# Kernel optimization log

Measured on AMD Instinct MI355X. Metric: run time of the kernel, lower is better.

The kernel has to match this reference:

```python
import jax, jax.numpy as jnp
import numpy as np

N_NODES = 10000
N_EDGES = 160000
D_IN = 128
D_EMB = 512
D_HID = 256
GAT_SLOPE = 0.2   # PyG GATv2Conv default negative_slope
MLP_SLOPE = 0.1   # relu_alpha


def _glorot(key, shape):
    fan_in, fan_out = shape[0], shape[-1]
    lim = np.sqrt(6.0 / (fan_in + fan_out))
    return jax.random.uniform(key, shape, jnp.float32, -lim, lim)


def setup_inputs() -> dict:
    key = jax.random.key(0)
    ks = jax.random.split(key, 20)
    inp = {
        'x': jax.random.normal(ks[0], (N_NODES, D_IN), jnp.float32),
        'edge_index': jax.random.randint(ks[1], (2, N_EDGES), 0, N_NODES, jnp.int64),
    }
    # GATv2 layers: (Wl, Wr, att, bias) each
    dims = [(D_IN, D_EMB), (D_EMB, D_EMB), (D_EMB, D_EMB)]
    for i, (di, do) in enumerate(dims, start=1):
        inp[f'Wl{i}'] = _glorot(ks[2 + 4 * i], (di, do))
        inp[f'Wr{i}'] = _glorot(ks[3 + 4 * i], (di, do))
        inp[f'att{i}'] = _glorot(ks[4 + 4 * i], (1, do))[0]
        inp[f'b{i}'] = jnp.zeros((do,), jnp.float32)
    # MLP
    inp['A1'] = _glorot(ks[2], (D_EMB, D_HID)); inp['c1'] = jnp.zeros((D_HID,), jnp.float32)
    inp['A2'] = _glorot(ks[3], (D_HID, D_HID)); inp['c2'] = jnp.zeros((D_HID,), jnp.float32)
    inp['A3'] = _glorot(ks[4], (D_HID, 1));     inp['c3'] = jnp.zeros((1,), jnp.float32)
    return inp


def gatv2_conv(x, src, dst, Wl, Wr, att, bias):
    # PyG GATv2Conv, heads=1: xl = source transform, xr = target transform
    xl = x @ Wl                                   # [N, D]
    xr = x @ Wr                                   # [N, D]
    # per-edge attention logit: att . leaky_relu(xl[src] + xr[dst])
    e = jax.nn.leaky_relu(xl[src] + xr[dst], GAT_SLOPE) @ att   # [E]
    # segment softmax over incoming edges of each dst node
    emax = jax.ops.segment_max(e, dst, num_segments=N_NODES)    # [N]
    w = jnp.exp(e - emax[dst])
    denom = jax.ops.segment_sum(w, dst, num_segments=N_NODES)   # [N]
    alpha = w / (denom[dst] + 1e-16)                             # [E]
    out = jax.ops.segment_sum(alpha[:, None] * xl[src], dst, num_segments=N_NODES)
    return out + bias


def reference(x, edge_index, Wl1, Wr1, att1, b1, Wl2, Wr2, att2, b2,
              Wl3, Wr3, att3, b3, A1, c1, A2, c2, A3, c3):
    src, dst = edge_index[0], edge_index[1]
    h = jnp.tanh(gatv2_conv(x, src, dst, Wl1, Wr1, att1, b1))
    h = jnp.tanh(gatv2_conv(h, src, dst, Wl2, Wr2, att2, b2))
    h = jnp.tanh(gatv2_conv(h, src, dst, Wl3, Wr3, att3, b3))
    h = jax.nn.leaky_relu(h @ A1 + c1, MLP_SLOPE)
    h = jax.nn.leaky_relu(h @ A2 + c2, MLP_SLOPE)
    logits = h @ A3 + c3                          # [N, 1]
    return jax.nn.softmax(logits, axis=0)         # softmax over nodes
```

## Files before the change

kernel.cpp:

```cpp
#include <hip/hip_runtime.h>
#include <hip/hip_bf16.h>

#define N_NODES 10000
#define N_EDGES 160000
#define D_IN    128
#define D_EMB   512
#define D_HID   256
#define DMAX    512

typedef unsigned short u16;
typedef __attribute__((ext_vector_type(8))) short short8;
typedef __attribute__((ext_vector_type(4))) float floatx4;

__device__ __forceinline__ float bf2f(u16 u) {
    union { unsigned int i; float f; } v; v.i = ((unsigned int)u) << 16; return v.f;
}
__device__ __forceinline__ u16 f2bf(float f) {
    union { float f; unsigned int i; } v; v.f = f;
    unsigned int x = v.i;
    return (u16)((x + 0x7fffu + ((x >> 16) & 1u)) >> 16);
}
__device__ __forceinline__ float inval(const void* p, int fp32, int idx) {
    return fp32 ? ((const float*)p)[idx] : bf2f(((const u16*)p)[idx]);
}

__device__ __forceinline__ void gld_lds16(const u16* g, u16* l) {
    __builtin_amdgcn_global_load_lds((const __attribute__((address_space(1))) void*)g,
                                     (__attribute__((address_space(3))) void*)l,
                                     16, 0, 0);
}

__device__ __forceinline__ int xcd_chunk(int bid, int total) {
    int q = total >> 3, r = total & 7;
    int xcd = bid & 7, idx = bid >> 3;
    return (xcd < r ? xcd * (q + 1) : r * (q + 1) + (xcd - r) * q) + idx;
}

__device__ __forceinline__ int edge_src(const int* __restrict__ ei, int flg, int e) {
    int v = flg ? ei[2 * e] : ei[e];
    return min(max(v, 0), N_NODES - 1);
}
__device__ __forceinline__ int edge_dst(const int* __restrict__ ei, int flg, int e) {
    int v = flg ? ei[2 * N_EDGES + 2 * e] : ei[N_EDGES + e];
    return min(max(v, 0), N_NODES - 1);
}

__global__ void sentinel_kernel(float* out, int n) {
    int i = blockIdx.x * 256 + threadIdx.x;
    if (i < n) out[i] = 1.0f;
}

__global__ __launch_bounds__(256)
void detect_zero_kernel(const int* __restrict__ ei, const u16* __restrict__ xu,
                        int* flag, int* counts, float* logits, int* ghist) {
    int gid = blockIdx.x * 256 + threadIdx.x;
    for (int i = gid; i < N_NODES; i += gridDim.x * 256) { counts[i] = 0; logits[i] = 0.f; }
    for (int i = gid; i < DMAX; i += gridDim.x * 256) ghist[i] = 0;
    if (blockIdx.x != 0) return;
    __shared__ int s_or[256];
    __shared__ int s_cnt[256];
    int t = threadIdx.x;
    int v = 0;
    for (int k = t; k < 4096; k += 256) v |= ei[1 + 2 * k];
    int c = 0;
    for (int k = t; k < 4096; k += 256) {
        u16 u = xu[k];
        int ex = (u >> 7) & 0xFF;
        bool plaus = (u == 0) || (ex >= 64 && ex <= 191);
        if (!plaus) c++;
    }
    s_or[t] = v; s_cnt[t] = c;
    __syncthreads();
    for (int off = 128; off > 0; off >>= 1) {
        if (t < off) { s_or[t] |= s_or[t + off]; s_cnt[t] += s_cnt[t + off]; }
        __syncthreads();
    }
    if (t == 0) {
        flag[0] = (s_or[0] == 0) ? 1 : 0;
        flag[1] = (s_cnt[0] > 256) ? 1 : 0;
    }
}

struct ConvJobs {
    const void* src[10];
    u16* dh[10];
    int rows[10], cols[10], trans[10];
    int cum[11];
    int njobs;
};

__global__ __launch_bounds__(256)
void convert_fused_kernel(ConvJobs jobs, const int* __restrict__ flag) {
    int idx = blockIdx.x * 256 + threadIdx.x;
    if (idx >= jobs.cum[jobs.njobs]) return;
    int fp32 = flag[1];
    int jb = 0;
    while (idx >= jobs.cum[jb + 1]) jb++;
    int local = idx - jobs.cum[jb];
    float v = inval(jobs.src[jb], fp32, local);
    u16 hi = f2bf(v);
    int o;
    if (jobs.trans[jb]) {
        int r = local / jobs.cols[jb], c = local % jobs.cols[jb];
        o = c * jobs.rows[jb] + r;
    } else o = local;
    jobs.dh[jb][o] = hi;
}

__global__ void count_edges_kernel(const int* __restrict__ ei, const int* __restrict__ flag,
                                   int* counts) {
    int e = blockIdx.x * 256 + threadIdx.x;
    if (e < N_EDGES) atomicAdd(&counts[edge_dst(ei, flag[0], e)], 1);
}

__global__ __launch_bounds__(256)
void scan_counts_kernel(int* counts, int* rowptr) {
    __shared__ int part[256];
    int tid = threadIdx.x;
    const int CH = 40;
    int base = tid * CH;
    int loc[CH];
    int s = 0;
    #pragma unroll
    for (int i = 0; i < CH; i++) {
        int idx = base + i;
        int c = (idx < N_NODES) ? counts[idx] : 0;
        loc[i] = s; s += c;
    }
    part[tid] = s;
    __syncthreads();
    for (int off = 1; off < 256; off <<= 1) {
        int v = part[tid];
        int add = (tid >= off) ? part[tid - off] : 0;
        __syncthreads();
        part[tid] = v + add;
        __syncthreads();
    }
    int pre = (tid > 0) ? part[tid - 1] : 0;
    #pragma unroll
    for (int i = 0; i < CH; i++) {
        int idx = base + i;
        if (idx < N_NODES) { int v = pre + loc[i]; rowptr[idx] = v; counts[idx] = v; }
    }
    if (tid == 255) rowptr[N_NODES] = part[255];
}

__global__ void fill_esrcp_kernel(const int* __restrict__ ei, const int* __restrict__ flag,
                                  int* counts, int* esrcp) {
    int e = blockIdx.x * 256 + threadIdx.x;
    if (e < N_EDGES) {
        int flg = flag[0];
        int pos = atomicAdd(&counts[edge_dst(ei, flg, e)], 1);
        if (pos >= 0 && pos < N_EDGES) esrcp[pos] = edge_src(ei, flg, e);
    }
}

__global__ __launch_bounds__(256)
void lpt_hist_kernel(const int* __restrict__ rowptr, int* __restrict__ ghist) {
    __shared__ int lhist[DMAX];
    int t = threadIdx.x;
    for (int d = t; d < DMAX; d += 256) lhist[d] = 0;
    __syncthreads();
    int n = blockIdx.x * 256 + t;
    if (n < N_NODES) {
        int d = min(rowptr[n + 1] - rowptr[n], DMAX - 1);
        atomicAdd(&lhist[d], 1);
    }
    __syncthreads();
    for (int d = t; d < DMAX; d += 256) {
        int c = lhist[d];
        if (c > 0) atomicAdd(&ghist[d], c);
    }
}

__global__ __launch_bounds__(256)
void lpt_scan_kernel(const int* __restrict__ ghist, int* __restrict__ doff) {
    __shared__ int part[256];
    int t = threadIdx.x;
    int d0 = (DMAX - 1) - 2 * t;
    int d1 = d0 - 1;
    int c0 = ghist[d0], c1 = ghist[d1];
    part[t] = c0 + c1;
    __syncthreads();
    for (int o = 1; o < 256; o <<= 1) {
        int v = part[t];
        int add = (t >= o) ? part[t - o] : 0;
        __syncthreads();
        part[t] = v + add;
        __syncthreads();
    }
    int pre = (t > 0) ? part[t - 1] : 0;
    doff[d0] = pre;
    doff[d1] = pre + c0;
}

__global__ __launch_bounds__(256)
void lpt_scatter_kernel(const int* __restrict__ rowptr, int* __restrict__ doff,
                        int* __restrict__ order) {
    __shared__ int lhist[DMAX];
    __shared__ int lbase[DMAX];
    int t = threadIdx.x;
    for (int d = t; d < DMAX; d += 256) lhist[d] = 0;
    __syncthreads();
    int n = blockIdx.x * 256 + t;
    int dg = 0;
    if (n < N_NODES) {
        dg = min(rowptr[n + 1] - rowptr[n], DMAX - 1);
        atomicAdd(&lhist[dg], 1);
    }
    __syncthreads();
    for (int d = t; d < DMAX; d += 256) {
        int c = lhist[d];
        lbase[d] = (c > 0) ? atomicAdd(&doff[d], c) : 0;
        lhist[d] = 0;
    }
    __syncthreads();
    if (n < N_NODES) {
        int rank = atomicAdd(&lhist[dg], 1);
        int pos = lbase[dg] + rank;
        if (pos >= 0 && pos < N_NODES) order[pos] = n;
    }
}

__global__ __launch_bounds__(256)
void gemm_dual_kernel(const u16* __restrict__ Ah,
                      const u16* __restrict__ B0h, const u16* __restrict__ B1h,
                      u16* __restrict__ C0, float* __restrict__ C1,
                      int M, int N, int K)
{
    __shared__ u16 sAh[2][128 * 32];
    __shared__ u16 sBh[2][128 * 32];
    int nb = N >> 7;
    int nx = 2 * nb;
    int ny = (M + 127) >> 7;
    int w = xcd_chunk((int)blockIdx.x, nx * ny);
    int by = w / nx;
    int bxh = w - by * nx;
    int half = bxh >= nb;
    int bx = half ? (bxh - nb) : bxh;
    const u16* BTh = half ? B1h : B0h;

    int tid = threadIdx.x;
    int lane = tid & 63, wv = tid >> 6;
    int l15 = lane & 15, l4 = lane >> 4;
    int wr = (wv >> 1) * 64, wc = (wv & 1) * 64;
    int m0 = by * 128, n0 = bx * 128;

    int i0 = tid, i1 = tid + 256;
    int r0 = i0 >> 2, b0 = i0 & 3, sb0 = b0 ^ ((r0 >> 1) & 3);
    int r1 = i1 >> 2, b1 = i1 & 3, sb1 = b1 ^ ((r1 >> 1) & 3);
    int gr0 = min(m0 + r0, M - 1), gr1 = min(m0 + r1, M - 1);
    const u16* a0p = Ah + (size_t)gr0 * K + sb0 * 8;
    const u16* a1p = Ah + (size_t)gr1 * K + sb1 * 8;
    const u16* bb0p = BTh + (size_t)(n0 + r0) * K + sb0 * 8;
    const u16* bb1p = BTh + (size_t)(n0 + r1) * K + sb1 * 8;
    int lo0 = wv * 64 * 8;
    int lo1 = (256 + wv * 64) * 8;

    floatx4 acc[4][4];
    #pragma unroll
    for (int i = 0; i < 4; i++)
        #pragma unroll
        for (int j = 0; j < 4; j++) acc[i][j] = (floatx4){0.f, 0.f, 0.f, 0.f};

    int aoff[4], boff[4];
    #pragma unroll
    for (int i = 0; i < 4; i++) {
        int arow = wr + i * 16 + l15;
        aoff[i] = arow * 32 + ((l4 ^ ((arow >> 1) & 3)) << 3);
        int bcol = wc + i * 16 + l15;
        boff[i] = bcol * 32 + ((l4 ^ ((bcol >> 1) & 3)) << 3);
    }

    for (int kk = 0; kk < K; kk += 64) {
        __syncthreads();
        gld_lds16(a0p + kk, &sAh[0][lo0]);
        gld_lds16(a1p + kk, &sAh[0][lo1]);
        gld_lds16(bb0p + kk, &sBh[0][lo0]);
        gld_lds16(bb1p + kk, &sBh[0][lo1]);
        gld_lds16(a0p + kk + 32, &sAh[1][lo0]);
        gld_lds16(a1p + kk + 32, &sAh[1][lo1]);
        gld_lds16(bb0p + kk + 32, &sBh[1][lo0]);
        gld_lds16(bb1p + kk + 32, &sBh[1][lo1]);
        __syncthreads();

        #pragma unroll
        for (int s = 0; s < 2; s++) {
            short8 ah[4];
            #pragma unroll
            for (int i = 0; i < 4; i++) ah[i] = *(const short8*)(&sAh[s][aoff[i]]);
            #pragma unroll
            for (int j = 0; j < 4; j++) {
                short8 bh = *(const short8*)(&sBh[s][boff[j]]);
                #pragma unroll
                for (int i = 0; i < 4; i++)
                    acc[i][j] = __builtin_amdgcn_mfma_f32_16x16x32_bf16(ah[i], bh, acc[i][j], 0, 0, 0);
            }
        }
    }

    #pragma unroll
    for (int j = 0; j < 4; j++) {
        int col = n0 + wc + j * 16 + l15;
        #pragma unroll
        for (int i = 0; i < 4; i++) {
            #pragma unroll
            for (int r = 0; r < 4; r++) {
                int row = m0 + wr + i * 16 + l4 * 4 + r;
                if (row < M) {
                    if (half) C1[(size_t)row * N + col] = acc[i][j][r];
                    else      C0[(size_t)row * N + col] = f2bf(acc[i][j][r]);
                }
            }
        }
    }
}

template<int FUSE>
__global__ __launch_bounds__(256)
void gemm_mlp64_kernel(const u16* __restrict__ Ah,
                       const u16* __restrict__ BTh,
                       u16* __restrict__ Ch,
                       const void* __restrict__ biasraw,
                       const void* __restrict__ A3raw, float* __restrict__ logits,
                       const int* __restrict__ flag,
                       int M, int N, int K)
{
    __shared__ u16 sAh[2][64 * 32];
    __shared__ u16 sBh[2][64 * 32];
    int tid = threadIdx.x;
    int lane = tid & 63, wv = tid >> 6;
    int l15 = lane & 15, l4 = lane >> 4;
    int nx = N >> 6;
    int ny = (M + 63) >> 6;
    int w = xcd_chunk((int)blockIdx.x, nx * ny);
    int by = w / nx;
    int bx = w - by * nx;
    int m0 = by * 64, n0 = bx * 64;

    int r = (tid >> 2), blk = tid & 3, sb = blk ^ ((r >> 1) & 3);
    int gr = min(m0 + r, M - 1);
    const u16* ap = Ah + (size_t)gr * K + sb * 8;
    const u16* bp = BTh + (size_t)(n0 + r) * K + sb * 8;
    int lo = wv * 64 * 8;

    floatx4 acc[4];
    #pragma unroll
    for (int j = 0; j < 4; j++) acc[j] = (floatx4){0.f, 0.f, 0.f, 0.f};

    int arow = wv * 16 + l15;
    int aoff = arow * 32 + ((l4 ^ ((arow >> 1) & 3)) << 3);
    int boff[4];
    #pragma unroll
    for (int j = 0; j < 4; j++) {
        int bcol = j * 16 + l15;
        boff[j] = bcol * 32 + ((l4 ^ ((bcol >> 1) & 3)) << 3);
    }

    for (int kk = 0; kk < K; kk += 64) {
        __syncthreads();
        gld_lds16(ap + kk, &sAh[0][lo]);
        gld_lds16(bp + kk, &sBh[0][lo]);
        gld_lds16(ap + kk + 32, &sAh[1][lo]);
        gld_lds16(bp + kk + 32, &sBh[1][lo]);
        __syncthreads();

        #pragma unroll
        for (int s = 0; s < 2; s++) {
            short8 ah = *(const short8*)(&sAh[s][aoff]);
            #pragma unroll
            for (int j = 0; j < 4; j++) {
                short8 bh = *(const short8*)(&sBh[s][boff[j]]);
                acc[j] = __builtin_amdgcn_mfma_f32_16x16x32_bf16(ah, bh, acc[j], 0, 0, 0);
            }
        }
    }

    const int fp32 = flag[1];
    float lsum[4] = {0.f, 0.f, 0.f, 0.f};
    #pragma unroll
    for (int j = 0; j < 4; j++) {
        int col = n0 + j * 16 + l15;
        float bv = inval(biasraw, fp32, col);
        float a3 = FUSE ? inval(A3raw, fp32, col) : 0.f;
        #pragma unroll
        for (int rr = 0; rr < 4; rr++) {
            int row = m0 + wv * 16 + l4 * 4 + rr;
            if (row < M) {
                float v = acc[j][rr] + bv;
                v = v > 0.f ? v : 0.1f * v;
                if (FUSE) {
                    lsum[rr] += v * a3;
                } else {
                    Ch[(size_t)row * N + col] = f2bf(v);
                }
            }
        }
    }
    if (FUSE) {
        #pragma unroll
        for (int rr = 0; rr < 4; rr++) {
            float s = lsum[rr];
            s += __shfl_xor(s, 1);
            s += __shfl_xor(s, 2);
            s += __shfl_xor(s, 4);
            s += __shfl_xor(s, 8);
            int row = m0 + wv * 16 + l4 * 4 + rr;
            if (l15 == 0 && row < M) atomicAdd(&logits[row], s);
        }
    }
}

__global__ __launch_bounds__(256)
void gat_wave_kernel(const int* __restrict__ rowptr, const int* __restrict__ esrcp,
                     const int* __restrict__ order,
                     const u16* __restrict__ xlb, const float* __restrict__ xr,
                     const void* __restrict__ att, const void* __restrict__ bias,
                     const int* __restrict__ flag,
                     u16* __restrict__ hh)
{
    int lane = threadIdx.x & 63, wv = threadIdx.x >> 6;
    int slot = blockIdx.x * 4 + wv;
    if (slot >= N_NODES) return;
    int n = order[slot];
    n = min(max(n, 0), N_NODES - 1);
    int fp32 = flag[1];
    int d0 = lane * 8;
    int l3 = lane & 3;

    int beg = rowptr[n], end = rowptr[n + 1];
    int deg = end - beg;
    int ng = (deg + 3) >> 2;

    const u16* xbase = xlb + d0;

    const float* xrr = xr + (size_t)n * D_EMB;
    float4 r0 = *(const float4*)(xrr + d0);
    float4 r1 = *(const float4*)(xrr + d0 + 4);
    float xrv[8] = {r0.x, r0.y, r0.z, r0.w, r1.x, r1.y, r1.z, r1.w};
    float attv[8];
    #pragma unroll
    for (int k = 0; k < 8; k++) attv[k] = inval(att, fp32, d0 + k);

    float m_run = -3.4e38f, s_run = 0.f;
    float acc[8] = {0.f, 0.f, 0.f, 0.f, 0.f, 0.f, 0.f, 0.f};

    auto ldidx = [&](int g) -> int {
        return esrcp[min(beg + 4 * g + l3, N_EDGES - 1)];
    };

    if (ng > 0) {
        int i0 = ldidx(0);
        uint4 cu0, cu1, cu2, cu3;
        {
            int s0 = __shfl(i0, 0), s1 = __shfl(i0, 1), s2 = __shfl(i0, 2), s3 = __shfl(i0, 3);
            cu0 = *(const uint4*)(xbase + (size_t)s0 * D_EMB);
            cu1 = *(const uint4*)(xbase + (size_t)s1 * D_EMB);
            cu2 = *(const uint4*)(xbase + (size_t)s2 * D_EMB);
            cu3 = *(const uint4*)(xbase + (size_t)s3 * D_EMB);
        }
        int nidx = (ng > 1) ? ldidx(1) : 0;

        for (int g = 0; g < ng; g++) {
            uint4 nu0, nu1, nu2, nu3;
            int nidx2 = 0;
            bool have_next = (g + 1 < ng);
            if (have_next) {
                int t0 = __shfl(nidx, 0), t1 = __shfl(nidx, 1),
                    t2 = __shfl(nidx, 2), t3 = __shfl(nidx, 3);
                nu0 = *(const uint4*)(xbase + (size_t)t0 * D_EMB);
                nu1 = *(const uint4*)(xbase + (size_t)t1 * D_EMB);
                nu2 = *(const uint4*)(xbase + (size_t)t2 * D_EMB);
                nu3 = *(const uint4*)(xbase + (size_t)t3 * D_EMB);
                if (g + 2 < ng) nidx2 = ldidx(g + 2);
            }

            union { uint4 q; u16 us[8]; } u0, u1, u2, u3;
            u0.q = cu0; u1.q = cu1; u2.q = cu2; u3.q = cu3;
            float v0[8], v1[8], v2[8], v3[8];
            #pragma unroll
            for (int k = 0; k < 8; k++) {
                v0[k] = bf2f(u0.us[k]); v1[k] = bf2f(u1.us[k]);
                v2[k] = bf2f(u2.us[k]); v3[k] = bf2f(u3.us[k]);
            }
            float e0 = 0.f, e1 = 0.f, e2 = 0.f, e3 = 0.f;
            #pragma unroll
            for (int k = 0; k < 8; k++) {
                float t0 = v0[k] + xrv[k]; t0 = fmaxf(t0, 0.2f * t0); e0 += attv[k] * t0;
                float t1 = v1[k] + xrv[k]; t1 = fmaxf(t1, 0.2f * t1); e1 += attv[k] * t1;
                float t2 = v2[k] + xrv[k]; t2 = fmaxf(t2, 0.2f * t2); e2 += attv[k] * t2;
                float t3 = v3[k] + xrv[k]; t3 = fmaxf(t3, 0.2f * t3); e3 += attv[k] * t3;
            }
            #pragma unroll
            for (int o = 32; o > 0; o >>= 1) {
                e0 += __shfl_xor(e0, o);
                e1 += __shfl_xor(e1, o);
                e2 += __shfl_xor(e2, o);
                e3 += __shfl_xor(e3, o);
            }
            int base = beg + 4 * g;
            if (base + 1 >= end) e1 = -3.4e38f;
            if (base + 2 >= end) e2 = -3.4e38f;
            if (base + 3 >= end) e3 = -3.4e38f;
            float m4 = fmaxf(fmaxf(e0, e1), fmaxf(e2, e3));
            float m_new = fmaxf(m_run, m4);
            float sc = __expf(m_run - m_new);
            float w0 = __expf(e0 - m_new), w1 = __expf(e1 - m_new);
            float w2 = __expf(e2 - m_new), w3 = __expf(e3 - m_new);
            s_run = s_run * sc + (w0 + w1) + (w2 + w3);
            #pragma unroll
            for (int k = 0; k < 8; k++)
                acc[k] = acc[k] * sc + w0 * v0[k] + w1 * v1[k] + w2 * v2[k] + w3 * v3[k];
            m_run = m_new;

            if (have_next) {
                cu0 = nu0; cu1 = nu1; cu2 = nu2; cu3 = nu3;
                nidx = nidx2;
            }
        }
    }

    float inv = 1.f / (s_run + 1e-16f);
    union { uint4 q; u16 us[8]; } ph;
    #pragma unroll
    for (int k = 0; k < 8; k++) {
        float h = tanhf(acc[k] * inv + inval(bias, fp32, d0 + k));
        ph.us[k] = f2bf(h);
    }
    *(uint4*)(&hh[(size_t)n * D_EMB + d0]) = ph.q;
}

__global__ __launch_bounds__(256)
void softmax_kernel(const float* __restrict__ logits, float* __restrict__ out)
{
    __shared__ float red[4];
    __shared__ float s_m, s_s;
    int tid = threadIdx.x, lane = tid & 63, wv = tid >> 6;
    float m = -3.4e38f;
    for (int i = tid; i < N_NODES; i += 256) m = fmaxf(m, logits[i]);
    #pragma unroll
    for (int o = 32; o > 0; o >>= 1) m = fmaxf(m, __shfl_down(m, o));
    if (lane == 0) red[wv] = m;
    __syncthreads();
    if (tid == 0) {
        float mm = red[0];
        for (int i = 1; i < 4; i++) mm = fmaxf(mm, red[i]);
        s_m = mm;
    }
    __syncthreads();
    float mm = s_m;
    float s = 0.f;
    for (int i = tid; i < N_NODES; i += 256) s += __expf(logits[i] - mm);
    #pragma unroll
    for (int o = 32; o > 0; o >>= 1) s += __shfl_down(s, o);
    if (lane == 0) red[wv] = s;
    __syncthreads();
    if (tid == 0) {
        float ss = 0.f;
        for (int i = 0; i < 4; i++) ss += red[i];
        s_s = ss;
    }
    __syncthreads();
    float invs = 1.f / s_s;
    for (int i = tid; i < N_NODES; i += 256) out[i] = __expf(logits[i] - mm) * invs;
}

extern "C" void kernel_launch(void* const* d_in, const int* in_sizes, int n_in,
                              void* d_out, int out_size, void* d_ws, size_t ws_size,
                              hipStream_t stream)
{
    const void* x   = d_in[0];
    const int*  ei  = (const int*)d_in[1];
    const void* Wl[3]  = {d_in[2],  d_in[6],  d_in[10]};
    const void* Wr[3]  = {d_in[3],  d_in[7],  d_in[11]};
    const void* att[3] = {d_in[4],  d_in[8],  d_in[12]};
    const void* bia[3] = {d_in[5],  d_in[9],  d_in[13]};
    const void* A1 = d_in[14];
    const void* c1 = d_in[15];
    const void* A2 = d_in[16];
    const void* c2 = d_in[17];
    const void* A3 = d_in[18];

    char* p = (char*)d_ws;
    auto alloc = [&](size_t bytes) {
        char* r = p;
        p += (bytes + 255) & ~(size_t)255;
        return r;
    };
    u16*   xlb    = (u16*)  alloc((size_t)N_NODES * D_EMB * 4);
    float* xr     = (float*)alloc((size_t)N_NODES * D_EMB * 4);
    u16*   hh     = (u16*)  alloc((size_t)N_NODES * D_EMB * 2);
    int*   esrcp  = (int*)  alloc((size_t)N_EDGES * 4);
    int*   rowptr = (int*)  alloc((size_t)(N_NODES + 1) * 4);
    int*   counts = (int*)  alloc((size_t)N_NODES * 4);
    int*   flag   = (int*)  alloc(256);
    float* logits = (float*)alloc((size_t)N_NODES * 4);
    int*   ghist  = (int*)  alloc(DMAX * 4);
    int*   doff   = (int*)  alloc(DMAX * 4);
    int*   order  = (int*)  alloc((size_t)N_NODES * 4);
    u16* wl1h = (u16*)alloc(D_EMB * D_IN  * 2);
    u16* wr1h = (u16*)alloc(D_EMB * D_IN  * 2);
    u16* wl2h = (u16*)alloc(D_EMB * D_EMB * 2);
    u16* wr2h = (u16*)alloc(D_EMB * D_EMB * 2);
    u16* wl3h = (u16*)alloc(D_EMB * D_EMB * 2);
    u16* wr3h = (u16*)alloc(D_EMB * D_EMB * 2);
    u16* a1h  = (u16*)alloc(D_EMB * D_HID * 2);
    u16* a2h  = (u16*)alloc(D_HID * D_HID * 2);
    u16* xph  = (u16*)alloc((size_t)N_NODES * D_IN * 2);
    size_t needed = (size_t)(p - (char*)d_ws);

    if (ws_size < needed) {
        sentinel_kernel<<<(out_size + 255) / 256, 256, 0, stream>>>((float*)d_out, out_size);
        return;
    }

    u16* m1h = (u16*)xlb;

    detect_zero_kernel<<<40, 256, 0, stream>>>(ei, (const u16*)x, flag, counts, logits, ghist);
    count_edges_kernel<<<(N_EDGES + 255) / 256, 256, 0, stream>>>(ei, flag, counts);
    scan_counts_kernel<<<1, 256, 0, stream>>>(counts, rowptr);
    fill_esrcp_kernel<<<(N_EDGES + 255) / 256, 256, 0, stream>>>(ei, flag, counts, esrcp);

    int nblk = (N_NODES + 255) / 256;
    lpt_hist_kernel<<<nblk, 256, 0, stream>>>(rowptr, ghist);
    lpt_scan_kernel<<<1, 256, 0, stream>>>(ghist, doff);
    lpt_scatter_kernel<<<nblk, 256, 0, stream>>>(rowptr, doff, order);

    ConvJobs jobs;
    auto setjob = [&](int i, const void* s, u16* dh, int r, int c, int tr) {
        jobs.src[i] = s; jobs.dh[i] = dh;
        jobs.rows[i] = r; jobs.cols[i] = c; jobs.trans[i] = tr;
    };
    setjob(0, x,     xph,  N_NODES, D_IN, 0);
    setjob(1, Wl[0], wl1h, D_IN,  D_EMB, 1);
    setjob(2, Wr[0], wr1h, D_IN,  D_EMB, 1);
    setjob(3, Wl[1], wl2h, D_EMB, D_EMB, 1);
    setjob(4, Wr[1], wr2h, D_EMB, D_EMB, 1);
    setjob(5, Wl[2], wl3h, D_EMB, D_EMB, 1);
    setjob(6, Wr[2], wr3h, D_EMB, D_EMB, 1);
    setjob(7, A1,    a1h,  D_EMB, D_HID, 1);
    setjob(8, A2,    a2h,  D_HID, D_HID, 1);
    jobs.njobs = 9;
    jobs.cum[0] = 0;
    for (int i = 0; i < 9; i++) jobs.cum[i + 1] = jobs.cum[i] + jobs.rows[i] * jobs.cols[i];
    int ctotal = jobs.cum[9];
    convert_fused_kernel<<<(ctotal + 255) / 256, 256, 0, stream>>>(jobs, flag);

    int gdual = (2 * D_EMB / 128) * ((N_NODES + 127) / 128);
    int gmlp  = (D_HID / 64) * ((N_NODES + 63) / 64);
    int gatgrid = (N_NODES + 3) / 4;

    gemm_dual_kernel<<<gdual, 256, 0, stream>>>(xph, wl1h, wr1h, xlb, xr, N_NODES, D_EMB, D_IN);
    gat_wave_kernel<<<gatgrid, 256, 0, stream>>>(rowptr, esrcp, order, xlb, xr, att[0], bia[0], flag, hh);
    gemm_dual_kernel<<<gdual, 256, 0, stream>>>(hh, wl2h, wr2h, xlb, xr, N_NODES, D_EMB, D_EMB);
    gat_wave_kernel<<<gatgrid, 256, 0, stream>>>(rowptr, esrcp, order, xlb, xr, att[1], bia[1], flag, hh);
    gemm_dual_kernel<<<gdual, 256, 0, stream>>>(hh, wl3h, wr3h, xlb, xr, N_NODES, D_EMB, D_EMB);
    gat_wave_kernel<<<gatgrid, 256, 0, stream>>>(rowptr, esrcp, order, xlb, xr, att[2], bia[2], flag, hh);

    gemm_mlp64_kernel<0><<<gmlp, 256, 0, stream>>>(hh, a1h, m1h, c1, nullptr, nullptr, flag, N_NODES, D_HID, D_EMB);
    gemm_mlp64_kernel<1><<<gmlp, 256, 0, stream>>>(m1h, a2h, nullptr, c2, A3, logits, flag, N_NODES, D_HID, D_HID);
    softmax_kernel<<<1, 256, 0, stream>>>(logits, (float*)d_out);
}
```

Before: 373.1 us.

## Merge CSR build and degree-sort preprocessing into fewer kernel launches

Folds edge counting into the weight-conversion kernel and computes the degree histogram and its scan inside the single-block count scan. The edge fill and LPT scatter now run as one launch with a block-index split. This cuts the preprocessing launches from eight to four (detect, count+convert, scan, fill+scatter), removing launch gaps and serialization. The cost is a longer single-block scan kernel with shared-memory atomics.

```diff
diff --git a/kernel.cpp b/kernel.cpp
--- a/kernel.cpp
+++ b/kernel.cpp
@@ -52,10 +52,9 @@
 
 __global__ __launch_bounds__(256)
 void detect_zero_kernel(const int* __restrict__ ei, const u16* __restrict__ xu,
-                        int* flag, int* counts, float* logits, int* ghist) {
+                        int* flag, int* counts, float* logits) {
     int gid = blockIdx.x * 256 + threadIdx.x;
     for (int i = gid; i < N_NODES; i += gridDim.x * 256) { counts[i] = 0; logits[i] = 0.f; }
-    for (int i = gid; i < DMAX; i += gridDim.x * 256) ghist[i] = 0;
     if (blockIdx.x != 0) return;
     __shared__ int s_or[256];
     __shared__ int s_cnt[256];
@@ -81,6 +80,8 @@
     }
 }
 
+#define EBLK ((N_EDGES + 255) / 256)
+
 struct ConvJobs {
     const void* src[10];
     u16* dh[10];
@@ -90,8 +91,15 @@
 };
 
 __global__ __launch_bounds__(256)
-void convert_fused_kernel(ConvJobs jobs, const int* __restrict__ flag) {
-    int idx = blockIdx.x * 256 + threadIdx.x;
+void count_convert_kernel(const int* __restrict__ ei, int* counts,
+                          ConvJobs jobs, const int* __restrict__ flag) {
+    int b = blockIdx.x;
+    if (b < EBLK) {
+        int e = b * 256 + threadIdx.x;
+        if (e < N_EDGES) atomicAdd(&counts[edge_dst(ei, flag[0], e)], 1);
+        return;
+    }
+    int idx = (b - EBLK) * 256 + threadIdx.x;
     if (idx >= jobs.cum[jobs.njobs]) return;
     int fp32 = flag[1];
     int jb = 0;
@@ -107,16 +115,13 @@
     jobs.dh[jb][o] = hi;
 }
 
-__global__ void count_edges_kernel(const int* __restrict__ ei, const int* __restrict__ flag,
-                                   int* counts) {
-    int e = blockIdx.x * 256 + threadIdx.x;
-    if (e < N_EDGES) atomicAdd(&counts[edge_dst(ei, flag[0], e)], 1);
-}
-
-__global__ __launch_bounds__(256)
-void scan_counts_kernel(int* counts, int* rowptr) {
+__global__ __launch_bounds__(256)
+void scan_counts_kernel(int* counts, int* rowptr, int* doff) {
     __shared__ int part[256];
+    __shared__ int hist[DMAX];
     int tid = threadIdx.x;
+    for (int d = tid; d < DMAX; d += 256) hist[d] = 0;
+    __syncthreads();
     const int CH = 40;
     int base = tid * CH;
     int loc[CH];
@@ -125,6 +130,7 @@
     for (int i = 0; i < CH; i++) {
         int idx = base + i;
         int c = (idx < N_NODES) ? counts[idx] : 0;
+        if (idx < N_NODES) atomicAdd(&hist[min(c, DMAX - 1)], 1);
         loc[i] = s; s += c;
     }
     part[tid] = s;
@@ -143,82 +149,62 @@
         if (idx < N_NODES) { int v = pre + loc[i]; rowptr[idx] = v; counts[idx] = v; }
     }
     if (tid == 255) rowptr[N_NODES] = part[255];
-}
-
-__global__ void fill_esrcp_kernel(const int* __restrict__ ei, const int* __restrict__ flag,
-                                  int* counts, int* esrcp) {
-    int e = blockIdx.x * 256 + threadIdx.x;
+    __syncthreads();
+    int d0 = (DMAX - 1) - 2 * tid;
+    int d1 = d0 - 1;
+    int c0 = hist[d0], c1 = hist[d1];
+    __syncthreads();
+    part[tid] = c0 + c1;
+    __syncthreads();
+    for (int o = 1; o < 256; o <<= 1) {
+        int v = part[tid];
+        int add = (tid >= o) ? part[tid - o] : 0;
+        __syncthreads();
+        part[tid] = v + add;
+        __syncthreads();
+    }
+    int pre2 = (tid > 0) ? part[tid - 1] : 0;
+    doff[d0] = pre2;
+    doff[d1] = pre2 + c0;
+}
+
+__global__ __launch_bounds__(256)
+void fill_scatter_kernel(const int* __restrict__ ei, const int* __restrict__ flag,
+                         const int* __restrict__ rowptr,
+                         int* counts, int* esrcp, int* doff, int* order) {
+    int b = blockIdx.x;
+    int nblk = (N_NODES + 255) / 256;
+    int t = threadIdx.x;
+    if (b < nblk) {
+        __shared__ int lhist[DMAX];
+        __shared__ int lbase[DMAX];
+        for (int d = t; d < DMAX; d += 256) lhist[d] = 0;
+        __syncthreads();
+        int n = b * 256 + t;
+        int dg = 0;
+        if (n < N_NODES) {
+            dg = min(rowptr[n + 1] - rowptr[n], DMAX - 1);
+            atomicAdd(&lhist[dg], 1);
+        }
+        __syncthreads();
+        for (int d = t; d < DMAX; d += 256) {
+            int c = lhist[d];
+            lbase[d] = (c > 0) ? atomicAdd(&doff[d], c) : 0;
+            lhist[d] = 0;
+        }
+        __syncthreads();
+        if (n < N_NODES) {
+            int rank = atomicAdd(&lhist[dg], 1);
+            int pos = lbase[dg] + rank;
+            if (pos >= 0 && pos < N_NODES) order[pos] = n;
+        }
+        return;
+    }
+    int e = (b - nblk) * 256 + t;
     if (e < N_EDGES) {
         int flg = flag[0];
         int pos = atomicAdd(&counts[edge_dst(ei, flg, e)], 1);
         if (pos >= 0 && pos < N_EDGES) esrcp[pos] = edge_src(ei, flg, e);
-    }
-}
-
-__global__ __launch_bounds__(256)
-void lpt_hist_kernel(const int* __restrict__ rowptr, int* __restrict__ ghist) {
-    __shared__ int lhist[DMAX];
-    int t = threadIdx.x;
-    for (int d = t; d < DMAX; d += 256) lhist[d] = 0;
-    __syncthreads();
-    int n = blockIdx.x * 256 + t;
-    if (n < N_NODES) {
-        int d = min(rowptr[n + 1] - rowptr[n], DMAX - 1);
-        atomicAdd(&lhist[d], 1);
-    }
-    __syncthreads();
-    for (int d = t; d < DMAX; d += 256) {
-        int c = lhist[d];
-        if (c > 0) atomicAdd(&ghist[d], c);
-    }
-}
-
-__global__ __launch_bounds__(256)
-void lpt_scan_kernel(const int* __restrict__ ghist, int* __restrict__ doff) {
-    __shared__ int part[256];
-    int t = threadIdx.x;
-    int d0 = (DMAX - 1) - 2 * t;
-    int d1 = d0 - 1;
-    int c0 = ghist[d0], c1 = ghist[d1];
-    part[t] = c0 + c1;
-    __syncthreads();
-    for (int o = 1; o < 256; o <<= 1) {
-        int v = part[t];
-        int add = (t >= o) ? part[t - o] : 0;
-        __syncthreads();
-        part[t] = v + add;
-        __syncthreads();
-    }
-    int pre = (t > 0) ? part[t - 1] : 0;
-    doff[d0] = pre;
-    doff[d1] = pre + c0;
-}
-
-__global__ __launch_bounds__(256)
-void lpt_scatter_kernel(const int* __restrict__ rowptr, int* __restrict__ doff,
-                        int* __restrict__ order) {
-    __shared__ int lhist[DMAX];
-    __shared__ int lbase[DMAX];
-    int t = threadIdx.x;
-    for (int d = t; d < DMAX; d += 256) lhist[d] = 0;
-    __syncthreads();
-    int n = blockIdx.x * 256 + t;
-    int dg = 0;
-    if (n < N_NODES) {
-        dg = min(rowptr[n + 1] - rowptr[n], DMAX - 1);
-        atomicAdd(&lhist[dg], 1);
-    }
-    __syncthreads();
-    for (int d = t; d < DMAX; d += 256) {
-        int c = lhist[d];
-        lbase[d] = (c > 0) ? atomicAdd(&doff[d], c) : 0;
-        lhist[d] = 0;
-    }
-    __syncthreads();
-    if (n < N_NODES) {
-        int rank = atomicAdd(&lhist[dg], 1);
-        int pos = lbase[dg] + rank;
-        if (pos >= 0 && pos < N_NODES) order[pos] = n;
     }
 }
 
@@ -595,7 +581,6 @@
     int*   counts = (int*)  alloc((size_t)N_NODES * 4);
     int*   flag   = (int*)  alloc(256);
     float* logits = (float*)alloc((size_t)N_NODES * 4);
-    int*   ghist  = (int*)  alloc(DMAX * 4);
     int*   doff   = (int*)  alloc(DMAX * 4);
     int*   order  = (int*)  alloc((size_t)N_NODES * 4);
     u16* wl1h = (u16*)alloc(D_EMB * D_IN  * 2);
@@ -616,15 +601,7 @@
 
     u16* m1h = (u16*)xlb;
 
-    detect_zero_kernel<<<40, 256, 0, stream>>>(ei, (const u16*)x, flag, counts, logits, ghist);
-    count_edges_kernel<<<(N_EDGES + 255) / 256, 256, 0, stream>>>(ei, flag, counts);
-    scan_counts_kernel<<<1, 256, 0, stream>>>(counts, rowptr);
-    fill_esrcp_kernel<<<(N_EDGES + 255) / 256, 256, 0, stream>>>(ei, flag, counts, esrcp);
-
-    int nblk = (N_NODES + 255) / 256;
-    lpt_hist_kernel<<<nblk, 256, 0, stream>>>(rowptr, ghist);
-    lpt_scan_kernel<<<1, 256, 0, stream>>>(ghist, doff);
-    lpt_scatter_kernel<<<nblk, 256, 0, stream>>>(rowptr, doff, order);
+    detect_zero_kernel<<<40, 256, 0, stream>>>(ei, (const u16*)x, flag, counts, logits);
 
     ConvJobs jobs;
     auto setjob = [&](int i, const void* s, u16* dh, int r, int c, int tr) {
@@ -644,7 +621,13 @@
     jobs.cum[0] = 0;
     for (int i = 0; i < 9; i++) jobs.cum[i + 1] = jobs.cum[i] + jobs.rows[i] * jobs.cols[i];
     int ctotal = jobs.cum[9];
-    convert_fused_kernel<<<(ctotal + 255) / 256, 256, 0, stream>>>(jobs, flag);
+    int convblk = (ctotal + 255) / 256;
+    count_convert_kernel<<<EBLK + convblk, 256, 0, stream>>>(ei, counts, jobs, flag);
+
+    scan_counts_kernel<<<1, 256, 0, stream>>>(counts, rowptr, doff);
+
+    int nblk = (N_NODES + 255) / 256;
+    fill_scatter_kernel<<<nblk + EBLK, 256, 0, stream>>>(ei, flag, rowptr, counts, esrcp, doff, order);
 
     int gdual = (2 * D_EMB / 128) * ((N_NODES + 127) / 128);
     int gmlp  = (D_HID / 64) * ((N_NODES + 63) / 64);
```

Result: faster. 365.4 us (-2.1%).
